# Kernel optimization log

Hardware: AMD Instinct MI355X
Metric: run time of the kernel (lower is better)

## Reference

```python
import jax, jax.numpy as jnp
import numpy as np

TOP_K = 2

def setup_inputs() -> dict:
    key = jax.random.key(0)
    k0, k1, k2, k3 = jax.random.split(key, 4)
    B, T, D, F, E = 2, 2048, 1024, 4096, 8
    x = jax.random.normal(k0, (B, T, D), dtype=jnp.float32)
    Wr = jax.random.normal(k1, (E, D), dtype=jnp.float32) * 0.02   # router weight [out=E, in=D]
    W1 = jax.random.normal(k2, (E, F, D), dtype=jnp.float32) * 0.02  # per-expert up-proj [out=F, in=D]
    W2 = jax.random.normal(k3, (E, D, F), dtype=jnp.float32) * 0.02  # per-expert down-proj [out=D, in=F]
    return {"x": x, "Wr": Wr, "W1": W1, "W2": W2}

def reference(x, Wr, W1, W2):
    B, T, D = x.shape
    E = Wr.shape[0]
    N = B * T
    xf = x.reshape(N, D)
    # Router in fp32 on the un-cast activations (as in the torch module).
    logits = xf @ Wr.T                                   # [N, E]
    probs = jax.nn.softmax(logits, axis=-1)
    topk_w, topk_idx = jax.lax.top_k(probs, TOP_K)       # [N, K]
    topk_w = topk_w / jnp.sum(topk_w, axis=-1, keepdims=True)
    # Combine weights scattered into a dense [N, E] dispatch/combine matrix
    # (top_k indices are distinct, so .set is exact).
    combine = jnp.zeros((N, E), dtype=jnp.float32)
    combine = combine.at[jnp.arange(N)[:, None], topk_idx].set(topk_w)
    # Expert FFN runs in bf16 (comm_dtype in the original all-to-all pipeline).
    xb = xf.astype(jnp.bfloat16)
    h = jax.nn.gelu(jnp.einsum('nd,efd->enf', xb, W1.astype(jnp.bfloat16)),
                    approximate=False)                   # [E, N, F]
    yo = jnp.einsum('enf,edf->end', h, W2.astype(jnp.bfloat16))  # [E, N, D]
    # Weighted combine: bf16 expert outputs * fp32 gate weights -> fp32 (torch promotion).
    out = jnp.einsum('end,ne->nd', yo.astype(jnp.float32), combine)
    return out.reshape(B, T, D)
```

## Files before the change

kernel.cpp:

```cpp
#include <hip/hip_runtime.h>
#include <hip/hip_bf16.h>

typedef __attribute__((ext_vector_type(8))) __bf16 bf16x8;
typedef __attribute__((ext_vector_type(4))) float floatx4;

constexpr int N_TOK = 4096;
constexpr int DDIM  = 1024;
constexpr int FDIM  = 4096;
constexpr int NEXP  = 8;
constexpr int NSLOT = 2 * N_TOK;
constexpr int MAXT  = 72;

static __device__ __forceinline__ unsigned short f2bf(float f) {
    union { __hip_bfloat16 h; unsigned short u; } v;
    v.h = __float2bfloat16(f);
    return v.u;
}

static __device__ __forceinline__ void gl2lds16(const unsigned short* g, unsigned short* l) {
    __builtin_amdgcn_global_load_lds(
        (__attribute__((address_space(1))) void*)g,
        (__attribute__((address_space(3))) void*)l,
        16, 0, 0);
}

__global__ void castX_kernel(const float* __restrict__ src, unsigned short* __restrict__ dst,
                             int* __restrict__ counts) {
    int i = blockIdx.x * 256 + threadIdx.x;
    float4 v = *(const float4*)(src + (size_t)i * 4);
    ushort4 o;
    o.x = f2bf(v.x); o.y = f2bf(v.y); o.z = f2bf(v.z); o.w = f2bf(v.w);
    *(ushort4*)(dst + (size_t)i * 4) = o;
    if (blockIdx.x == 0 && threadIdx.x < NEXP) counts[threadIdx.x] = 0;
}

__global__ void castW_kernel(const float* __restrict__ W1, const float* __restrict__ W2,
                             unsigned short* __restrict__ w1b, unsigned short* __restrict__ w2b) {
    constexpr int HALF = NEXP * FDIM * DDIM / 4;
    int i = blockIdx.x * 256 + threadIdx.x;
    const float* s; unsigned short* d; int j;
    if (i < HALF) { s = W1; d = w1b; j = i; }
    else          { s = W2; d = w2b; j = i - HALF; }
    float4 v = *(const float4*)(s + (size_t)j * 4);
    ushort4 o;
    o.x = f2bf(v.x); o.y = f2bf(v.y); o.z = f2bf(v.z); o.w = f2bf(v.w);
    *(ushort4*)(d + (size_t)j * 4) = o;
}

__global__ void router_kernel(const float* __restrict__ x, const float* __restrict__ Wr,
                              int* __restrict__ te, float* __restrict__ tw,
                              int* __restrict__ counts) {
    __shared__ float wr[NEXP * DDIM];
    const int tid = threadIdx.x;
    for (int i = tid; i < NEXP * DDIM; i += 256) wr[i] = Wr[i];
    __syncthreads();
    const int wave = tid >> 6, lane = tid & 63;
    const int t = blockIdx.x * 4 + wave;

    float xr[16];
    const float* xp = x + (size_t)t * DDIM;
    #pragma unroll
    for (int i = 0; i < 16; i++) xr[i] = xp[lane + 64 * i];

    float logit[NEXP];
    #pragma unroll
    for (int e = 0; e < NEXP; e++) {
        float s = 0.f;
        #pragma unroll
        for (int i = 0; i < 16; i++) s += xr[i] * wr[e * DDIM + lane + 64 * i];
        #pragma unroll
        for (int off = 32; off > 0; off >>= 1) s += __shfl_xor(s, off, 64);
        logit[e] = s;
    }
    if (lane == 0) {
        int i0 = 0; float l0 = logit[0];
        #pragma unroll
        for (int e = 1; e < NEXP; e++) if (logit[e] > l0) { l0 = logit[e]; i0 = e; }
        int i1 = -1; float l1 = -3.0e38f;
        #pragma unroll
        for (int e = 0; e < NEXP; e++) if (e != i0 && logit[e] > l1) { l1 = logit[e]; i1 = e; }
        float p1 = expf(l1 - l0);
        float w0 = 1.f / (1.f + p1);
        float w1 = p1 * w0;
        te[t * 2] = i0; te[t * 2 + 1] = i1;
        tw[t * 2] = w0; tw[t * 2 + 1] = w1;
        atomicAdd(&counts[i0], 1);
        atomicAdd(&counts[i1], 1);
    }
}

__global__ void scan_scatter_kernel(const int* __restrict__ counts,
                                    const int* __restrict__ te, const float* __restrict__ tw,
                                    int* __restrict__ offsets, int* __restrict__ tile_em,
                                    int* __restrict__ ntile,
                                    int* __restrict__ rowid, float* __restrict__ gate,
                                    int* __restrict__ tok2slot) {
    __shared__ int soff[NEXP];
    __shared__ int scur[NEXP];
    const int tid = threadIdx.x;
    if (tid == 0) {
        int acc = 0, nt = 0;
        for (int e = 0; e < NEXP; e++) {
            offsets[e] = acc; soff[e] = acc;
            for (int m0 = 0; m0 < counts[e]; m0 += 128)
                tile_em[nt++] = (e << 16) | (m0 >> 7);
            acc += counts[e];
        }
        offsets[NEXP] = acc;
        ntile[0] = nt;
        for (int i = nt; i < MAXT; i++) tile_em[i] = 0;
    }
    if (tid < NEXP) scur[tid] = 0;
    __syncthreads();
    for (int t = tid; t < N_TOK; t += 256) {
        #pragma unroll
        for (int k = 0; k < 2; k++) {
            int e = te[t * 2 + k];
            int pos = atomicAdd(&scur[e], 1);
            int slot = soff[e] + pos;
            rowid[slot] = t;
            gate[slot] = tw[t * 2 + k];
            tok2slot[t * 2 + k] = slot;
        }
    }
}

template <int K, bool UP>
__global__ __launch_bounds__(256)
void ffn_gemm(const unsigned short* __restrict__ A,
              const unsigned short* __restrict__ Wb,
              unsigned short* __restrict__ Hout,
              float* __restrict__ Y,
              const int* __restrict__ rowid,
              const float* __restrict__ gate,
              const int* __restrict__ offsets,
              const int* __restrict__ tile_em,
              const int* __restrict__ ntile) {
    constexpr int BM = 128, BN = 128, BK = 64;
    constexpr int NOUT  = UP ? FDIM : DDIM;
    constexpr int NSLAB = (NOUT / BN) / 8;

    const int id    = blockIdx.x;
    const int xcd   = id & 7;
    const int local = id >> 3;
    const int nloc  = local / MAXT;
    const int bt    = local - nloc * MAXT;
    if (bt >= ntile[0]) return;
    const int em = tile_em[bt];
    const int e  = em >> 16;
    const int m0 = (em & 0xffff) << 7;
    const int n0 = (xcd * NSLAB + nloc) * BN;
    const int seg = offsets[e];
    const int cnt = offsets[e + 1] - seg;

    __shared__ __align__(16) unsigned short As[BM * BK];
    __shared__ __align__(16) unsigned short Bs[BN * BK];

    const int tid  = threadIdx.x;
    const int lane = tid & 63;
    const int wave = tid >> 6;

    const int rl   = lane >> 3;
    const int cg   = (lane & 7) ^ rl;

    const unsigned short* ag[4];
    #pragma unroll
    for (int j = 0; j < 4; j++) {
        int r = wave * 32 + j * 8 + rl;
        int slot = seg + m0 + r;
        if (slot >= NSLOT) slot = NSLOT - 1;
        if (UP) { int t = rowid[slot]; ag[j] = A + (size_t)t * DDIM + cg * 8; }
        else    { ag[j] = A + (size_t)slot * FDIM + cg * 8; }
    }
    const unsigned short* bg[4];
    #pragma unroll
    for (int j = 0; j < 4; j++) {
        int r = wave * 32 + j * 8 + rl;
        bg[j] = Wb + ((size_t)e * NOUT + n0 + r) * K + cg * 8;
    }
    unsigned short* asl[4];
    unsigned short* bsl[4];
    #pragma unroll
    for (int j = 0; j < 4; j++) {
        asl[j] = &As[(wave * 32 + j * 8) * BK] + lane * 8;
        bsl[j] = &Bs[(wave * 32 + j * 8) * BK] + lane * 8;
    }

    const int wm = (wave >> 1) * 64;
    const int wn = (wave & 1) * 64;
    const int frow = lane & 15;
    const int quad = lane >> 4;
    const int f7 = frow & 7;

    floatx4 acc[4][4];
    #pragma unroll
    for (int i = 0; i < 4; i++)
        #pragma unroll
        for (int j = 0; j < 4; j++)
            acc[i][j] = (floatx4){0.f, 0.f, 0.f, 0.f};

    for (int k0 = 0; k0 < K; k0 += BK) {
        __syncthreads();
        #pragma unroll
        for (int j = 0; j < 4; j++) gl2lds16(ag[j], asl[j]);
        #pragma unroll
        for (int j = 0; j < 4; j++) gl2lds16(bg[j], bsl[j]);
        #pragma unroll
        for (int j = 0; j < 4; j++) { ag[j] += BK; bg[j] += BK; }
        __syncthreads();

        #pragma unroll
        for (int kk = 0; kk < 2; kk++) {
            bf16x8 av[4], bv[4];
            #pragma unroll
            for (int i = 0; i < 4; i++)
                av[i] = *(const bf16x8*)&As[(wm + i * 16 + frow) * BK + ((kk * 4 + quad) ^ f7) * 8];
            #pragma unroll
            for (int i = 0; i < 4; i++)
                bv[i] = *(const bf16x8*)&Bs[(wn + i * 16 + frow) * BK + ((kk * 4 + quad) ^ f7) * 8];
            #pragma unroll
            for (int mt = 0; mt < 4; mt++)
                #pragma unroll
                for (int nt = 0; nt < 4; nt++)
                    acc[mt][nt] = __builtin_amdgcn_mfma_f32_16x16x32_bf16(av[mt], bv[nt], acc[mt][nt], 0, 0, 0);
        }
    }

    #pragma unroll
    for (int mt = 0; mt < 4; mt++) {
        #pragma unroll
        for (int r = 0; r < 4; r++) {
            int mloc = m0 + wm + mt * 16 + quad * 4 + r;
            if (mloc >= cnt) continue;
            int slot = seg + mloc;
            if (UP) {
                #pragma unroll
                for (int nt = 0; nt < 4; nt++) {
                    int n = n0 + wn + nt * 16 + frow;
                    float v = acc[mt][nt][r];
                    float g = 0.5f * v * (1.0f + erff(v * 0.70710678118654752f));
                    Hout[(size_t)slot * FDIM + n] = f2bf(g);
                }
            } else {
                float gw = gate[slot];
                #pragma unroll
                for (int nt = 0; nt < 4; nt++) {
                    int n = n0 + wn + nt * 16 + frow;
                    Y[(size_t)slot * DDIM + n] = gw * acc[mt][nt][r];
                }
            }
        }
    }
}

__global__ void combine_kernel(const float* __restrict__ Y, const int* __restrict__ tok2slot,
                               float* __restrict__ out) {
    int idx = blockIdx.x * 256 + threadIdx.x;
    int t = idx >> 8;
    int c = (idx & 255) * 4;
    int s0 = tok2slot[t * 2], s1 = tok2slot[t * 2 + 1];
    float4 a = *(const float4*)(Y + (size_t)s0 * DDIM + c);
    float4 b = *(const float4*)(Y + (size_t)s1 * DDIM + c);
    *(float4*)(out + (size_t)t * DDIM + c) =
        make_float4(a.x + b.x, a.y + b.y, a.z + b.z, a.w + b.w);
}

extern "C" void kernel_launch(void* const* d_in, const int* in_sizes, int n_in,
                              void* d_out, int out_size, void* d_ws, size_t ws_size,
                              hipStream_t stream) {
    const float* x  = (const float*)d_in[0];
    const float* Wr = (const float*)d_in[1];
    const float* W1 = (const float*)d_in[2];
    const float* W2 = (const float*)d_in[3];
    float* out = (float*)d_out;

    char* ws = (char*)d_ws;
    size_t off = 0;
    auto alloc = [&](size_t bytes) -> char* {
        char* p = ws + off;
        off = (off + bytes + 255) & ~(size_t)255;
        return p;
    };
    unsigned short* xb   = (unsigned short*)alloc((size_t)N_TOK * DDIM * 2);
    unsigned short* H    = (unsigned short*)alloc((size_t)NSLOT * FDIM * 2);
    float* Yb      = (float*)alloc((size_t)NSLOT * DDIM * 4);
    int*   rowid   = (int*)alloc(NSLOT * 4);
    float* gatew   = (float*)alloc(NSLOT * 4);
    int*   te      = (int*)alloc(NSLOT * 4);
    float* tw      = (float*)alloc(NSLOT * 4);
    int*   t2s     = (int*)alloc(NSLOT * 4);
    int*   counts  = (int*)alloc(64);
    int*   offsets = (int*)alloc(64);
    int*   tile_em = (int*)alloc(MAXT * 4);
    int*   ntile   = (int*)alloc(64);
    unsigned short* w1b = (unsigned short*)alloc((size_t)NEXP * FDIM * DDIM * 2);
    unsigned short* w2b = (unsigned short*)alloc((size_t)NEXP * DDIM * FDIM * 2);
    (void)ws_size;

    castX_kernel<<<N_TOK * DDIM / 4 / 256, 256, 0, stream>>>(x, xb, counts);
    castW_kernel<<<2 * NEXP * FDIM * DDIM / 4 / 256, 256, 0, stream>>>(W1, W2, w1b, w2b);
    router_kernel<<<N_TOK / 4, 256, 0, stream>>>(x, Wr, te, tw, counts);
    scan_scatter_kernel<<<1, 256, 0, stream>>>(counts, te, tw, offsets, tile_em, ntile,
                                               rowid, gatew, t2s);
    ffn_gemm<DDIM, true ><<<8 * 4 * MAXT, 256, 0, stream>>>(xb, w1b, H, Yb, rowid, gatew,
                                                            offsets, tile_em, ntile);
    ffn_gemm<FDIM, false><<<8 * 1 * MAXT, 256, 0, stream>>>(H,  w2b, H, Yb, rowid, gatew,
                                                            offsets, tile_em, ntile);
    combine_kernel<<<N_TOK, 256, 0, stream>>>(Yb, t2s, out);
}
```

Measured before the change: 712.7 us.

## Split-K the down-projection, fuse x cast into router, shrink GEMM K-tile

The down-projection GEMM is split along K into two halves writing separate partial buffers that the combine kernel sums, giving it more blocks to fill the GPU. The bf16 cast of x moves into the router kernel, removing one launch and a second read of x. The GEMM K-tile drops from 64 to 32 without the XOR swizzle, and the XCD-aware block mapping becomes a plain linear mapping. The smaller tile and missing swizzle may add LDS bank conflicts and sync overhead per MFMA, and the split doubles the Y buffer traffic.

```diff
diff --git a/kernel.cpp b/kernel.cpp
--- a/kernel.cpp
+++ b/kernel.cpp
@@ -10,6 +10,9 @@
 constexpr int NEXP  = 8;
 constexpr int NSLOT = 2 * N_TOK;
 constexpr int MAXT  = 72;
+constexpr int KSPLIT = 2;
+constexpr int NN_UP = FDIM / 128;
+constexpr int NN_DN = DDIM / 128;
 
 static __device__ __forceinline__ unsigned short f2bf(float f) {
     union { __hip_bfloat16 h; unsigned short u; } v;
@@ -24,18 +27,9 @@
         16, 0, 0);
 }
 
-__global__ void castX_kernel(const float* __restrict__ src, unsigned short* __restrict__ dst,
+__global__ void castW_kernel(const float* __restrict__ W1, const float* __restrict__ W2,
+                             unsigned short* __restrict__ w1b, unsigned short* __restrict__ w2b,
                              int* __restrict__ counts) {
-    int i = blockIdx.x * 256 + threadIdx.x;
-    float4 v = *(const float4*)(src + (size_t)i * 4);
-    ushort4 o;
-    o.x = f2bf(v.x); o.y = f2bf(v.y); o.z = f2bf(v.z); o.w = f2bf(v.w);
-    *(ushort4*)(dst + (size_t)i * 4) = o;
-    if (blockIdx.x == 0 && threadIdx.x < NEXP) counts[threadIdx.x] = 0;
-}
-
-__global__ void castW_kernel(const float* __restrict__ W1, const float* __restrict__ W2,
-                             unsigned short* __restrict__ w1b, unsigned short* __restrict__ w2b) {
     constexpr int HALF = NEXP * FDIM * DDIM / 4;
     int i = blockIdx.x * 256 + threadIdx.x;
     const float* s; unsigned short* d; int j;
@@ -45,9 +39,11 @@
     ushort4 o;
     o.x = f2bf(v.x); o.y = f2bf(v.y); o.z = f2bf(v.z); o.w = f2bf(v.w);
     *(ushort4*)(d + (size_t)j * 4) = o;
+    if (blockIdx.x == 0 && threadIdx.x < NEXP) counts[threadIdx.x] = 0;
 }
 
 __global__ void router_kernel(const float* __restrict__ x, const float* __restrict__ Wr,
+                              unsigned short* __restrict__ xb,
                               int* __restrict__ te, float* __restrict__ tw,
                               int* __restrict__ counts) {
     __shared__ float wr[NEXP * DDIM];
@@ -61,6 +57,10 @@
     const float* xp = x + (size_t)t * DDIM;
     #pragma unroll
     for (int i = 0; i < 16; i++) xr[i] = xp[lane + 64 * i];
+
+    unsigned short* xbp = xb + (size_t)t * DDIM;
+    #pragma unroll
+    for (int i = 0; i < 16; i++) xbp[lane + 64 * i] = f2bf(xr[i]);
 
     float logit[NEXP];
     #pragma unroll
@@ -125,7 +125,7 @@
     }
 }
 
-template <int K, bool UP>
+template <bool UP>
 __global__ __launch_bounds__(256)
 void ffn_gemm(const unsigned short* __restrict__ A,
               const unsigned short* __restrict__ Wb,
@@ -136,61 +136,61 @@
               const int* __restrict__ offsets,
               const int* __restrict__ tile_em,
               const int* __restrict__ ntile) {
-    constexpr int BM = 128, BN = 128, BK = 64;
-    constexpr int NOUT  = UP ? FDIM : DDIM;
-    constexpr int NSLAB = (NOUT / BN) / 8;
-
-    const int id    = blockIdx.x;
-    const int xcd   = id & 7;
-    const int local = id >> 3;
-    const int nloc  = local / MAXT;
-    const int bt    = local - nloc * MAXT;
+    constexpr int BM = 128, BN = 128, BK = 32, LDT = 32;
+    constexpr int NOUT = UP ? FDIM : DDIM;
+    constexpr int KDIM = UP ? DDIM : FDIM;
+    constexpr int NN   = UP ? NN_UP : NN_DN;
+    constexpr int KLEN = UP ? DDIM : (FDIM / KSPLIT);
+
+    const int id = blockIdx.x;
+    const int n0 = (id % NN) * BN;
+    const int bt = (id / NN) % MAXT;
+    const int ks = UP ? 0 : (id / (NN * MAXT));
     if (bt >= ntile[0]) return;
     const int em = tile_em[bt];
     const int e  = em >> 16;
     const int m0 = (em & 0xffff) << 7;
-    const int n0 = (xcd * NSLAB + nloc) * BN;
     const int seg = offsets[e];
     const int cnt = offsets[e + 1] - seg;
-
-    __shared__ __align__(16) unsigned short As[BM * BK];
-    __shared__ __align__(16) unsigned short Bs[BN * BK];
+    const int kbase = ks * KLEN;
+
+    __shared__ __align__(16) unsigned short As[BM * LDT];
+    __shared__ __align__(16) unsigned short Bs[BN * LDT];
 
     const int tid  = threadIdx.x;
     const int lane = tid & 63;
     const int wave = tid >> 6;
 
-    const int rl   = lane >> 3;
-    const int cg   = (lane & 7) ^ rl;
-
-    const unsigned short* ag[4];
-    #pragma unroll
-    for (int j = 0; j < 4; j++) {
-        int r = wave * 32 + j * 8 + rl;
+    const int srow0 = wave * 32 + (lane >> 2);
+    const int chunk = lane & 3;
+
+    const unsigned short* ag[2];
+    #pragma unroll
+    for (int j = 0; j < 2; j++) {
+        int r = srow0 + j * 16;
         int slot = seg + m0 + r;
         if (slot >= NSLOT) slot = NSLOT - 1;
-        if (UP) { int t = rowid[slot]; ag[j] = A + (size_t)t * DDIM + cg * 8; }
-        else    { ag[j] = A + (size_t)slot * FDIM + cg * 8; }
-    }
-    const unsigned short* bg[4];
-    #pragma unroll
-    for (int j = 0; j < 4; j++) {
-        int r = wave * 32 + j * 8 + rl;
-        bg[j] = Wb + ((size_t)e * NOUT + n0 + r) * K + cg * 8;
-    }
-    unsigned short* asl[4];
-    unsigned short* bsl[4];
-    #pragma unroll
-    for (int j = 0; j < 4; j++) {
-        asl[j] = &As[(wave * 32 + j * 8) * BK] + lane * 8;
-        bsl[j] = &Bs[(wave * 32 + j * 8) * BK] + lane * 8;
+        if (UP) { int t = rowid[slot]; ag[j] = A + (size_t)t * DDIM + kbase + chunk * 8; }
+        else    { ag[j] = A + (size_t)slot * FDIM + kbase + chunk * 8; }
+    }
+    const unsigned short* bg[2];
+    #pragma unroll
+    for (int j = 0; j < 2; j++) {
+        int r = srow0 + j * 16;
+        bg[j] = Wb + ((size_t)e * NOUT + n0 + r) * KDIM + kbase + chunk * 8;
+    }
+    unsigned short* asl[2];
+    unsigned short* bsl[2];
+    #pragma unroll
+    for (int j = 0; j < 2; j++) {
+        asl[j] = &As[(wave * 32 + j * 16) * LDT] + lane * 8;
+        bsl[j] = &Bs[(wave * 32 + j * 16) * LDT] + lane * 8;
     }
 
     const int wm = (wave >> 1) * 64;
     const int wn = (wave & 1) * 64;
     const int frow = lane & 15;
     const int quad = lane >> 4;
-    const int f7 = frow & 7;
 
     floatx4 acc[4][4];
     #pragma unroll
@@ -199,31 +199,27 @@
         for (int j = 0; j < 4; j++)
             acc[i][j] = (floatx4){0.f, 0.f, 0.f, 0.f};
 
-    for (int k0 = 0; k0 < K; k0 += BK) {
+    for (int k0 = 0; k0 < KLEN; k0 += BK) {
         __syncthreads();
-        #pragma unroll
-        for (int j = 0; j < 4; j++) gl2lds16(ag[j], asl[j]);
-        #pragma unroll
-        for (int j = 0; j < 4; j++) gl2lds16(bg[j], bsl[j]);
-        #pragma unroll
-        for (int j = 0; j < 4; j++) { ag[j] += BK; bg[j] += BK; }
+        gl2lds16(ag[0], asl[0]);
+        gl2lds16(ag[1], asl[1]);
+        gl2lds16(bg[0], bsl[0]);
+        gl2lds16(bg[1], bsl[1]);
+        ag[0] += BK; ag[1] += BK; bg[0] += BK; bg[1] += BK;
         __syncthreads();
 
-        #pragma unroll
-        for (int kk = 0; kk < 2; kk++) {
-            bf16x8 av[4], bv[4];
+        bf16x8 av[4], bv[4];
+        #pragma unroll
+        for (int i = 0; i < 4; i++)
+            av[i] = *(const bf16x8*)&As[(wm + i * 16 + frow) * LDT + quad * 8];
+        #pragma unroll
+        for (int i = 0; i < 4; i++)
+            bv[i] = *(const bf16x8*)&Bs[(wn + i * 16 + frow) * LDT + quad * 8];
+        #pragma unroll
+        for (int mt = 0; mt < 4; mt++)
             #pragma unroll
-            for (int i = 0; i < 4; i++)
-                av[i] = *(const bf16x8*)&As[(wm + i * 16 + frow) * BK + ((kk * 4 + quad) ^ f7) * 8];
-            #pragma unroll
-            for (int i = 0; i < 4; i++)
-                bv[i] = *(const bf16x8*)&Bs[(wn + i * 16 + frow) * BK + ((kk * 4 + quad) ^ f7) * 8];
-            #pragma unroll
-            for (int mt = 0; mt < 4; mt++)
-                #pragma unroll
-                for (int nt = 0; nt < 4; nt++)
-                    acc[mt][nt] = __builtin_amdgcn_mfma_f32_16x16x32_bf16(av[mt], bv[nt], acc[mt][nt], 0, 0, 0);
-        }
+            for (int nt = 0; nt < 4; nt++)
+                acc[mt][nt] = __builtin_amdgcn_mfma_f32_16x16x32_bf16(av[mt], bv[nt], acc[mt][nt], 0, 0, 0);
     }
 
     #pragma unroll
@@ -246,7 +242,7 @@
                 #pragma unroll
                 for (int nt = 0; nt < 4; nt++) {
                     int n = n0 + wn + nt * 16 + frow;
-                    Y[(size_t)slot * DDIM + n] = gw * acc[mt][nt][r];
+                    Y[((size_t)ks * NSLOT + slot) * DDIM + n] = gw * acc[mt][nt][r];
                 }
             }
         }
@@ -259,10 +255,14 @@
     int t = idx >> 8;
     int c = (idx & 255) * 4;
     int s0 = tok2slot[t * 2], s1 = tok2slot[t * 2 + 1];
-    float4 a = *(const float4*)(Y + (size_t)s0 * DDIM + c);
-    float4 b = *(const float4*)(Y + (size_t)s1 * DDIM + c);
-    *(float4*)(out + (size_t)t * DDIM + c) =
-        make_float4(a.x + b.x, a.y + b.y, a.z + b.z, a.w + b.w);
+    float4 r = make_float4(0.f, 0.f, 0.f, 0.f);
+    #pragma unroll
+    for (int ks = 0; ks < KSPLIT; ks++) {
+        float4 a = *(const float4*)(Y + ((size_t)ks * NSLOT + s0) * DDIM + c);
+        float4 b = *(const float4*)(Y + ((size_t)ks * NSLOT + s1) * DDIM + c);
+        r.x += a.x + b.x; r.y += a.y + b.y; r.z += a.z + b.z; r.w += a.w + b.w;
+    }
+    *(float4*)(out + (size_t)t * DDIM + c) = r;
 }
 
 extern "C" void kernel_launch(void* const* d_in, const int* in_sizes, int n_in,
@@ -283,7 +283,7 @@
     };
     unsigned short* xb   = (unsigned short*)alloc((size_t)N_TOK * DDIM * 2);
     unsigned short* H    = (unsigned short*)alloc((size_t)NSLOT * FDIM * 2);
-    float* Yb      = (float*)alloc((size_t)NSLOT * DDIM * 4);
+    float* Yb      = (float*)alloc((size_t)KSPLIT * NSLOT * DDIM * 4);
     int*   rowid   = (int*)alloc(NSLOT * 4);
     float* gatew   = (float*)alloc(NSLOT * 4);
     int*   te      = (int*)alloc(NSLOT * 4);
@@ -297,14 +297,13 @@
     unsigned short* w2b = (unsigned short*)alloc((size_t)NEXP * DDIM * FDIM * 2);
     (void)ws_size;
 
-    castX_kernel<<<N_TOK * DDIM / 4 / 256, 256, 0, stream>>>(x, xb, counts);
-    castW_kernel<<<2 * NEXP * FDIM * DDIM / 4 / 256, 256, 0, stream>>>(W1, W2, w1b, w2b);
-    router_kernel<<<N_TOK / 4, 256, 0, stream>>>(x, Wr, te, tw, counts);
+    castW_kernel<<<2 * NEXP * FDIM * DDIM / 4 / 256, 256, 0, stream>>>(W1, W2, w1b, w2b, counts);
+    router_kernel<<<N_TOK / 4, 256, 0, stream>>>(x, Wr, xb, te, tw, counts);
     scan_scatter_kernel<<<1, 256, 0, stream>>>(counts, te, tw, offsets, tile_em, ntile,
                                                rowid, gatew, t2s);
-    ffn_gemm<DDIM, true ><<<8 * 4 * MAXT, 256, 0, stream>>>(xb, w1b, H, Yb, rowid, gatew,
-                                                            offsets, tile_em, ntile);
-    ffn_gemm<FDIM, false><<<8 * 1 * MAXT, 256, 0, stream>>>(H,  w2b, H, Yb, rowid, gatew,
-                                                            offsets, tile_em, ntile);
+    ffn_gemm<true ><<<NN_UP * MAXT, 256, 0, stream>>>(xb, w1b, H, Yb, rowid, gatew,
+                                                      offsets, tile_em, ntile);
+    ffn_gemm<false><<<NN_DN * MAXT * KSPLIT, 256, 0, stream>>>(H, w2b, H, Yb, rowid, gatew,
+                                                               offsets, tile_em, ntile);
     combine_kernel<<<N_TOK, 256, 0, stream>>>(Yb, t2s, out);
 }
```

Result: faster. 668.6 us (-6.2%).
